# Optimization experiments

Measured on AMD Instinct MI355X. Metric: run time of the kernel, lower is better.

Reference implementation:

```python
import jax, jax.numpy as jnp
import numpy as np
import math

B, C, H, W = 8, 512, 32, 32
NUM_GROUPS = 32
NUM_HEADS = C // 64  # num_head_channels=64 -> 8 heads
EPS = 1e-5


def setup_inputs() -> dict:
    key = jax.random.key(0)
    ks = jax.random.split(key, 7)
    x = jax.random.normal(ks[0], (B, C, H, W), dtype=jnp.float32)
    gn_w = jax.random.uniform(ks[1], (C,), dtype=jnp.float32, minval=0.5, maxval=1.5)
    gn_b = jax.random.normal(ks[2], (C,), dtype=jnp.float32) * 0.1
    qkv_w = jax.random.normal(ks[3], (3 * C, C), dtype=jnp.float32) * 0.02
    qkv_b = jax.random.normal(ks[4], (3 * C,), dtype=jnp.float32) * 0.02
    proj_w = jax.random.normal(ks[5], (C, C), dtype=jnp.float32) * 0.02
    proj_b = jax.random.normal(ks[6], (C,), dtype=jnp.float32) * 0.02
    return {"x": x, "gn_w": gn_w, "gn_b": gn_b, "qkv_w": qkv_w,
            "qkv_b": qkv_b, "proj_w": proj_w, "proj_b": proj_b}


def _group_norm(x, w, b):
    # x: [B, C, L]
    bb, cc, ll = x.shape
    g = x.reshape(bb, NUM_GROUPS, cc // NUM_GROUPS, ll)
    mean = g.mean(axis=(2, 3), keepdims=True)
    var = g.var(axis=(2, 3), keepdims=True)
    g = (g - mean) * jax.lax.rsqrt(var + EPS)
    return g.reshape(bb, cc, ll) * w[None, :, None] + b[None, :, None]


def reference(x, gn_w, gn_b, qkv_w, qkv_b, proj_w, proj_b):
    b, c, h, w = x.shape
    L = h * w
    xf = x.reshape(b, c, L)
    # 1x1 conv1d QKV on normalized input: weight [3C, C]
    qkv = jnp.einsum('oc,bcl->bol', qkv_w, _group_norm(xf, gn_w, gn_b)) + qkv_b[None, :, None]
    ch = c // NUM_HEADS  # per-head channels
    qkv = qkv.reshape(b * NUM_HEADS, 3 * ch, L)
    q, k, v = qkv[:, :ch], qkv[:, ch:2 * ch], qkv[:, 2 * ch:]
    scale = 1.0 / math.sqrt(math.sqrt(ch))
    # [b*H, T, S] scores, softmax over source dim (computed in fp32 per source)
    weight = jnp.einsum('bct,bcs->bts', q * scale, k * scale)
    weight = jax.nn.softmax(weight.astype(jnp.float32), axis=-1).astype(weight.dtype)
    a = jnp.einsum('bts,bcs->bct', weight, v).reshape(b, c, L)
    hproj = jnp.einsum('oc,bcl->bol', proj_w, a) + proj_b[None, :, None]
    return (xf + hproj).reshape(b, c, h, w)
```

## Files before the change

### kernel.cpp

```cpp
#include <hip/hip_runtime.h>
#include <math.h>

#define BB 8
#define CC 512
#define LL 1024
#define GG 32
#define CPG 16
#define NH 8
#define CH 64

typedef unsigned short ushort_t;
typedef __attribute__((ext_vector_type(8))) short short8;
typedef __attribute__((ext_vector_type(4))) float f32x4;
typedef __attribute__((ext_vector_type(16))) float f32x16;

#define SCALE_Q 0.18033688f

__device__ inline ushort_t f2bf(float f) {
  union { float f; unsigned u; } v;
  v.f = f;
  unsigned r = v.u + 0x7FFFu + ((v.u >> 16) & 1u);
  return (ushort_t)(r >> 16);
}

__device__ inline unsigned pack_bf2(float lo, float hi) {
  return __builtin_amdgcn_perm(__float_as_uint(hi), __float_as_uint(lo),
                               0x07060302u);
}

__device__ inline int swz(int r, int k) {
  return r * 64 + ((((k >> 3) ^ (r & 7)) << 3) | (k & 7));
}

__device__ __forceinline__ void g2l16(const void* g, void* l) {
  __builtin_amdgcn_global_load_lds((const unsigned int*)g, (unsigned int*)l,
                                   16, 0, 0);
}

__global__ __launch_bounds__(512) void gnx_kernel(
    const float* __restrict__ x, const float* __restrict__ gn_w,
    const float* __restrict__ gn_b, const float* __restrict__ qkv_w,
    const float* __restrict__ proj_w, ushort_t* __restrict__ xnT,
    ushort_t* __restrict__ wq, ushort_t* __restrict__ wp) {
  if (blockIdx.x < BB * GG) {
    const int b = blockIdx.x / GG;
    const int g = blockIdx.x % GG;
    const int tid = threadIdx.x;
    const int ch = tid >> 5;
    const int lseg = tid & 31;
    __shared__ ushort_t Ts[1024 * 32];
    __shared__ float red[16];
    __shared__ float st[2];
    const float* xc = x + ((size_t)b * CC + (size_t)g * CPG + ch) * LL;
    float4 v[8];
    float sum = 0.f, sq = 0.f;
#pragma unroll
    for (int i = 0; i < 8; ++i) {
      v[i] = *(const float4*)(xc + lseg * 32 + i * 4);
      sum += (v[i].x + v[i].y) + (v[i].z + v[i].w);
      sq += (v[i].x * v[i].x + v[i].y * v[i].y) +
            (v[i].z * v[i].z + v[i].w * v[i].w);
    }
#pragma unroll
    for (int off = 32; off > 0; off >>= 1) {
      sum += __shfl_down(sum, off);
      sq += __shfl_down(sq, off);
    }
    const int wave = tid >> 6;
    if ((tid & 63) == 0) {
      red[wave] = sum;
      red[8 + wave] = sq;
    }
    __syncthreads();
    if (tid == 0) {
      float s = 0.f, q = 0.f;
#pragma unroll
      for (int i = 0; i < 8; ++i) {
        s += red[i];
        q += red[8 + i];
      }
      float mean = s * (1.f / (CPG * LL));
      float var = q * (1.f / (CPG * LL)) - mean * mean;
      st[0] = mean;
      st[1] = rsqrtf(var + 1e-5f);
    }
    __syncthreads();
    const int c = g * CPG + ch;
    const float sc = st[1] * gn_w[c];
    const float sh = gn_b[c] - st[0] * sc;
    const int chG = ch >> 3, ch7 = ch & 7;
#pragma unroll
    for (int i = 0; i < 8; ++i) {
      float vv[4] = {v[i].x, v[i].y, v[i].z, v[i].w};
#pragma unroll
      for (int j = 0; j < 4; ++j) {
        int l = lseg * 32 + i * 4 + j;
        int key = ((l >> 5) + (l >> 2)) & 3;
        int slot = (chG + key) & 3;
        Ts[l * 32 + slot * 8 + ch7] = f2bf(vv[j] * sc + sh);
      }
    }
    __syncthreads();
    const int cb64 = (g >> 2) * 64;
    const int grpb = (g & 3) * 2;
#pragma unroll
    for (int it = 0; it < 4; ++it) {
      int idx = tid + it * 512;
      int l = idx >> 1, gsel = idx & 1;
      int key = ((l >> 5) + (l >> 2)) & 3;
      int slot = (gsel + key) & 3;
      uint4 val = *(const uint4*)&Ts[l * 32 + slot * 8];
      int grp = (grpb + gsel) ^ (l & 7);
      *(uint4*)(xnT + ((size_t)b * LL + l) * CC + cb64 + grp * 8) = val;
    }
  } else {
    int cb = blockIdx.x - BB * GG;
    int idx = (cb * 512 + threadIdx.x) * 4;
    const int N1 = 3 * CC * CC;
    float4 v;
    ushort_t* mat;
    int row, k;
    if (idx < N1) {
      v = *(const float4*)(qkv_w + idx);
      row = idx >> 9;
      k = idx & 511;
      mat = wq + (size_t)row * CC;
    } else {
      int j = idx - N1;
      v = *(const float4*)(proj_w + j);
      row = j >> 9;
      k = j & 511;
      mat = wp + (size_t)row * CC;
    }
    int dcol = (k & ~63) | ((((k >> 3) & 7) ^ (row & 7)) << 3) | (k & 7);
    unsigned lo = f2bf(v.x) | ((unsigned)f2bf(v.y) << 16);
    unsigned hi = f2bf(v.z) | ((unsigned)f2bf(v.w) << 16);
    *(uint2*)(mat + dcol) = make_uint2(lo, hi);
  }
}

__global__ __launch_bounds__(384, 3) void qkv_mfma_kernel(
    const ushort_t* __restrict__ wq, const ushort_t* __restrict__ xnT,
    const float* __restrict__ qkv_b, ushort_t* __restrict__ qT,
    ushort_t* __restrict__ kT, ushort_t* __restrict__ vbuf) {
  const int b = blockIdx.z;
  const int m0 = blockIdx.y * 192;
  const int n0 = blockIdx.x * 128;
  const int tid = threadIdx.x;
  const int w = tid >> 6, lane = tid & 63;
  const int col = lane & 15, quad = lane >> 4;
  const int wm = (w >> 1) * 64, wn = (w & 1) * 64;
  __shared__ ushort_t Smem[2 * 20480];
  f32x4 acc[4][4];
  f32x4 z = {0.f, 0.f, 0.f, 0.f};
#pragma unroll
  for (int i = 0; i < 4; ++i)
#pragma unroll
    for (int j = 0; j < 4; ++j) acc[i][j] = z;

  const ushort_t* arow = wq + (size_t)m0 * CC;
  const ushort_t* brow = xnT + ((size_t)b * LL + n0) * CC;

  auto stage = [&](int bb, int k0) {
    ushort_t* As = Smem + bb * 20480;
    ushort_t* Bs = As + 12288;
#pragma unroll
    for (int j = 0; j < 4; ++j) {
      int e = (j * 6 + w) * 512 + lane * 8;
      g2l16(arow + (size_t)(e >> 6) * CC + k0 + (e & 63),
            As + (j * 6 + w) * 512);
    }
    if (w < 4) {
#pragma unroll
      for (int j = 0; j < 4; ++j) {
        int e = (j * 4 + w) * 512 + lane * 8;
        g2l16(brow + (size_t)(e >> 6) * CC + k0 + (e & 63),
              Bs + (j * 4 + w) * 512);
      }
    }
  };

  stage(0, 0);
  __syncthreads();
  int cur = 0;
  for (int step = 0; step < 8; ++step) {
    if (step < 7) stage(cur ^ 1, (step + 1) * 64);
    const ushort_t* As = Smem + cur * 20480;
    const ushort_t* Bs = As + 12288;
#pragma unroll
    for (int kk = 0; kk < 2; ++kk) {
      short8 af[4], bf[4];
#pragma unroll
      for (int mi = 0; mi < 4; ++mi)
        af[mi] = *(const short8*)&As[swz(wm + mi * 16 + col, kk * 32 + quad * 8)];
#pragma unroll
      for (int ni = 0; ni < 4; ++ni)
        bf[ni] = *(const short8*)&Bs[swz(wn + ni * 16 + col, kk * 32 + quad * 8)];
#pragma unroll
      for (int mi = 0; mi < 4; ++mi)
#pragma unroll
        for (int ni = 0; ni < 4; ++ni)
          acc[mi][ni] = __builtin_amdgcn_mfma_f32_16x16x32_bf16(
              af[mi], bf[ni], acc[mi][ni], 0, 0, 0);
    }
    __syncthreads();
    cur ^= 1;
  }
  const int ci_w = w >> 1;
  ushort_t* Tile = Smem + ci_w * 8192;
  if (ci_w < 2) {
    const float sc = (ci_w == 0) ? SCALE_Q : 1.f;
#pragma unroll
    for (int mi = 0; mi < 4; ++mi) {
      int mg = m0 + wm + mi * 16 + quad * 4;
      float b0 = qkv_b[mg + 0], b1 = qkv_b[mg + 1];
      float b2 = qkv_b[mg + 2], b3 = qkv_b[mg + 3];
      int ch = mi * 16 + quad * 4;
#pragma unroll
      for (int ni = 0; ni < 4; ++ni) {
        int lloc = wn + ni * 16 + col;
        float v0 = (acc[mi][ni][0] + b0) * sc;
        float v1 = (acc[mi][ni][1] + b1) * sc;
        float v2 = (acc[mi][ni][2] + b2) * sc;
        float v3 = (acc[mi][ni][3] + b3) * sc;
        int chs = ch ^ ((lloc & 7) << 3);
        *(uint2*)&Tile[lloc * 64 + chs] =
            make_uint2(pack_bf2(v0, v1), pack_bf2(v2, v3));
      }
    }
  } else {
#pragma unroll
    for (int mi = 0; mi < 4; ++mi)
#pragma unroll
      for (int r = 0; r < 4; ++r) {
        int ch = mi * 16 + quad * 4 + r;
        float bias = qkv_b[m0 + wm + ch];
#pragma unroll
        for (int ni = 0; ni < 4; ++ni) {
          int lloc = wn + ni * 16 + col;
          Tile[ch * 128 + lloc] =
              (ushort_t)(__float_as_uint(acc[mi][ni][r] + bias) >> 16);
        }
      }
  }
  __syncthreads();
  const int head = blockIdx.y;
  const int bh = b * NH + head;
#pragma unroll
  for (int ci = 0; ci < 3; ++ci) {
    ushort_t* T2 = Smem + ci * 8192;
    if (ci < 2) {
      ushort_t* dst = (ci == 0) ? qT : kT;
#pragma unroll
      for (int it = 0; it < 3; ++it) {
        int idx = tid + it * 384;
        if (idx < 1024) {
          int l = idx >> 3, seg = idx & 7;
          uint4 v = *(const uint4*)&T2[l * 64 + seg * 8];
          *(uint4*)(dst + ((size_t)bh * LL + n0 + l) * CH + seg * 8) = v;
        }
      }
    } else {
#pragma unroll
      for (int it = 0; it < 3; ++it) {
        int idx = tid + it * 384;
        if (idx < 1024) {
          int ch = idx >> 4, lseg = idx & 15;
          uint4 v = *(const uint4*)&T2[ch * 128 + lseg * 8];
          int g = lseg & 7, blk = lseg >> 3;
          *(uint4*)(vbuf + ((size_t)bh * CH + ch) * LL + n0 + blk * 64 +
                    ((g ^ (ch & 7)) << 3)) = v;
        }
      }
    }
  }
}

__global__ __launch_bounds__(512) void attn_mfma_kernel(
    const ushort_t* __restrict__ qT, const ushort_t* __restrict__ kT,
    const ushort_t* __restrict__ vbuf, ushort_t* __restrict__ abuf) {
  const int Bx = blockIdx.x;
  const int bh = (Bx & 7) * 8 + ((Bx >> 3) >> 2);
  const int t0g = ((Bx >> 3) & 3) * 256;
  const int b = bh >> 3, h = bh & 7;
  const int tid = threadIdx.x;
  const int w = tid >> 6, lane = tid & 63;
  const int ln31 = lane & 31, hi = lane >> 5;
  __shared__ ushort_t Ksm[2][64 * 64];
  __shared__ ushort_t Vsm[2][64 * 64];

  const ushort_t* kbase = kT + (size_t)bh * LL * CH;
  const ushort_t* vbase = vbuf + (size_t)bh * CH * LL;
  const int eb = w * 512 + lane * 8;

  g2l16(kbase + eb, &Ksm[0][w * 512]);
  g2l16(vbase + (size_t)(eb >> 6) * LL + (eb & 63), &Vsm[0][w * 512]);
  const ushort_t* qtile = qT + ((size_t)bh * LL + t0g) * CH;
  short8 bq[4];
#pragma unroll
  for (int j = 0; j < 4; ++j)
    bq[j] = *(const short8*)&qtile[swz(w * 32 + ln31, j * 16 + hi * 8)];

  float m_s = 0.f, lsum = 0.f;
  f32x16 oacc[2];
  f32x16 zz = {0.f, 0.f, 0.f, 0.f, 0.f, 0.f, 0.f, 0.f,
               0.f, 0.f, 0.f, 0.f, 0.f, 0.f, 0.f, 0.f};
  oacc[0] = zz;
  oacc[1] = zz;
  __syncthreads();

  int cur = 0;
  for (int it = 0; it < 16; ++it) {
    if (it < 15) {
      g2l16(kbase + (size_t)(it + 1) * 64 * CH + eb, &Ksm[cur ^ 1][w * 512]);
      g2l16(vbase + (size_t)(eb >> 6) * LL + (it + 1) * 64 + (eb & 63),
            &Vsm[cur ^ 1][w * 512]);
    }
    const ushort_t* Kc = Ksm[cur];
    const ushort_t* Vc = Vsm[cur];
    f32x16 sacc[2];
    sacc[0] = zz;
    sacc[1] = zz;
    __builtin_amdgcn_s_setprio(1);
#pragma unroll
    for (int sq = 0; sq < 2; ++sq)
#pragma unroll
      for (int j = 0; j < 4; ++j) {
        short8 ak = *(const short8*)&Kc[swz(sq * 32 + ln31, j * 16 + hi * 8)];
        sacc[sq] = __builtin_amdgcn_mfma_f32_32x32x16_bf16(ak, bq[j],
                                                           sacc[sq], 0, 0, 0);
      }
    __builtin_amdgcn_s_setprio(0);
    if (it == 0) {
      float mx = sacc[0][0];
#pragma unroll
      for (int sq = 0; sq < 2; ++sq)
#pragma unroll
        for (int r = 0; r < 16; ++r) mx = fmaxf(mx, sacc[sq][r]);
#pragma unroll
      for (int off = 32; off > 0; off >>= 1) mx = fmaxf(mx, __shfl_xor(mx, off));
      m_s = mx;
    }
    short8 pf[4];
#pragma unroll
    for (int sq = 0; sq < 2; ++sq) {
      float p[16];
#pragma unroll
      for (int r = 0; r < 16; ++r) {
        p[r] = __builtin_amdgcn_exp2f(sacc[sq][r] - m_s);
        lsum += p[r];
      }
      unsigned d0[4], d1[4];
#pragma unroll
      for (int q = 0; q < 4; ++q) {
        d0[q] = pack_bf2(p[q * 4 + 0], p[q * 4 + 1]);
        d1[q] = pack_bf2(p[q * 4 + 2], p[q * 4 + 3]);
      }
#pragma unroll
      for (int m = 0; m < 2; ++m) {
        unsigned x0 = d0[m * 2], y0 = d0[m * 2 + 1];
        unsigned x1 = d1[m * 2], y1 = d1[m * 2 + 1];
        asm volatile("v_permlane32_swap_b32 %0, %1" : "+v"(x0), "+v"(y0));
        asm volatile("v_permlane32_swap_b32 %0, %1" : "+v"(x1), "+v"(y1));
        union { uint4 u; short8 s; } fu;
        fu.u = make_uint4(x0, x1, y0, y1);
        pf[sq * 2 + m] = fu.s;
      }
    }
    __builtin_amdgcn_s_setprio(1);
#pragma unroll
    for (int cq = 0; cq < 2; ++cq)
#pragma unroll
      for (int ks = 0; ks < 4; ++ks) {
        short8 bv = *(const short8*)&Vc[swz(cq * 32 + ln31, ks * 16 + hi * 8)];
        oacc[cq] = __builtin_amdgcn_mfma_f32_32x32x16_bf16(pf[ks], bv,
                                                           oacc[cq], 0, 0, 0);
      }
    __builtin_amdgcn_s_setprio(0);
    __syncthreads();
    cur ^= 1;
  }
  lsum += __shfl_xor(lsum, 32);
#pragma unroll
  for (int r = 0; r < 16; ++r) {
    int tl = (r & 3) + 8 * (r >> 2) + 4 * hi;
    float li = 1.f / __shfl(lsum, tl, 64);
    int lg = t0g + w * 32 + tl;
#pragma unroll
    for (int cq = 0; cq < 2; ++cq) {
      int cl = cq * 32 + ln31;
      int dcol = ((((cl >> 3) ^ (lg & 7)) << 3) | (cl & 7));
      abuf[((size_t)b * LL + lg) * CC + h * CH + dcol] =
          f2bf(oacc[cq][r] * li);
    }
  }
}

__global__ __launch_bounds__(256) void proj_mfma_kernel(
    const ushort_t* __restrict__ wp, const ushort_t* __restrict__ abuf,
    const float* __restrict__ proj_b, const float* __restrict__ x,
    float* __restrict__ out) {
  const int b = blockIdx.z;
  const int m0 = blockIdx.y * 64;
  const int n0 = blockIdx.x * 128;
  const int tid = threadIdx.x;
  const int w = tid >> 6, lane = tid & 63;
  const int col = lane & 15, quad = lane >> 4;
  const int wm = (w >> 1) * 32, wn = (w & 1) * 64;
  __shared__ ushort_t Smem[2 * 12288];
  f32x4 acc[2][4];
  f32x4 z = {0.f, 0.f, 0.f, 0.f};
#pragma unroll
  for (int i = 0; i < 2; ++i)
#pragma unroll
    for (int j = 0; j < 4; ++j) acc[i][j] = z;

  const ushort_t* arow = wp + (size_t)m0 * CC;
  const ushort_t* brow = abuf + ((size_t)b * LL + n0) * CC;

  auto stage = [&](int bb, int k0) {
    ushort_t* As = Smem + bb * 12288;
    ushort_t* Bs = As + 4096;
#pragma unroll
    for (int j = 0; j < 2; ++j) {
      int e = (j * 4 + w) * 512 + lane * 8;
      g2l16(arow + (size_t)(e >> 6) * CC + k0 + (e & 63),
            As + (j * 4 + w) * 512);
    }
#pragma unroll
    for (int j = 0; j < 4; ++j) {
      int e = (j * 4 + w) * 512 + lane * 8;
      g2l16(brow + (size_t)(e >> 6) * CC + k0 + (e & 63),
            Bs + (j * 4 + w) * 512);
    }
  };

  stage(0, 0);
  __syncthreads();
  int cur = 0;
  for (int step = 0; step < 8; ++step) {
    if (step < 7) stage(cur ^ 1, (step + 1) * 64);
    const ushort_t* As = Smem + cur * 12288;
    const ushort_t* Bs = As + 4096;
#pragma unroll
    for (int kk = 0; kk < 2; ++kk) {
      short8 af[2], bf[4];
#pragma unroll
      for (int mi = 0; mi < 2; ++mi)
        af[mi] = *(const short8*)&As[swz(wm + mi * 16 + col, kk * 32 + quad * 8)];
#pragma unroll
      for (int ni = 0; ni < 4; ++ni)
        bf[ni] = *(const short8*)&Bs[swz(wn + ni * 16 + col, kk * 32 + quad * 8)];
#pragma unroll
      for (int mi = 0; mi < 2; ++mi)
#pragma unroll
        for (int ni = 0; ni < 4; ++ni)
          acc[mi][ni] = __builtin_amdgcn_mfma_f32_16x16x32_bf16(
              af[mi], bf[ni], acc[mi][ni], 0, 0, 0);
    }
    __syncthreads();
    cur ^= 1;
  }
#pragma unroll
  for (int mi = 0; mi < 2; ++mi)
#pragma unroll
    for (int r = 0; r < 4; ++r) {
      int o = m0 + wm + mi * 16 + quad * 4 + r;
      float bias = proj_b[o];
#pragma unroll
      for (int ni = 0; ni < 4; ++ni) {
        int l = n0 + wn + ni * 16 + col;
        size_t off = ((size_t)b * CC + o) * LL + l;
        out[off] = x[off] + bias + acc[mi][ni][r];
      }
    }
}

extern "C" void kernel_launch(void* const* d_in, const int* in_sizes, int n_in,
                              void* d_out, int out_size, void* d_ws,
                              size_t ws_size, hipStream_t stream) {
  const float* x = (const float*)d_in[0];
  const float* gn_w = (const float*)d_in[1];
  const float* gn_b = (const float*)d_in[2];
  const float* qkv_w = (const float*)d_in[3];
  const float* qkv_b = (const float*)d_in[4];
  const float* proj_w = (const float*)d_in[5];
  const float* proj_b = (const float*)d_in[6];
  float* out = (float*)d_out;

  char* ws = (char*)d_ws;
  ushort_t* wq = (ushort_t*)ws;
  ushort_t* wp = wq + (size_t)3 * CC * CC;
  ushort_t* xnT = wp + (size_t)CC * CC;
  ushort_t* qT = xnT + (size_t)BB * LL * CC;
  ushort_t* kT = qT + (size_t)BB * NH * LL * CH;
  ushort_t* vb = kT + (size_t)BB * NH * LL * CH;
  ushort_t* abuf = vb + (size_t)BB * NH * LL * CH;

  gnx_kernel<<<BB * GG + 512, 512, 0, stream>>>(x, gn_w, gn_b, qkv_w, proj_w,
                                                xnT, wq, wp);
  qkv_mfma_kernel<<<dim3(LL / 128, 1536 / 192, BB), 384, 0, stream>>>(
      wq, xnT, qkv_b, qT, kT, vb);
  attn_mfma_kernel<<<dim3(256), 512, 0, stream>>>(qT, kT, vb, abuf);
  proj_mfma_kernel<<<dim3(LL / 128, CC / 64, BB), 256, 0, stream>>>(
      wp, abuf, proj_b, x, out);
}
```

Baseline: 140.1 us.

## Retile attention to 128-query blocks with 128-key stages and MFMA row sums

The attention kernel now runs 512 blocks of 4 waves, each covering 128 queries, instead of 256 blocks of 8 waves. Each pipeline stage double-buffers a 128-key K/V tile, so there are half as many barriers per block. V tiles are addressed with a new 128-wide swizzle that matches the existing 64-element swizzle in the V buffer. The softmax denominator is now computed by an extra MFMA against a vector of bf16 ones rather than scalar adds and shuffles. This adds about a quarter more matrix work and doubles global K/V reads per head, in exchange for more blocks, fewer syncs and less VALU work.

```diff
diff --git a/kernel.cpp b/kernel.cpp
--- a/kernel.cpp
+++ b/kernel.cpp
@@ -30,6 +30,10 @@
 
 __device__ inline int swz(int r, int k) {
   return r * 64 + ((((k >> 3) ^ (r & 7)) << 3) | (k & 7));
+}
+
+__device__ inline int vswz(int c, int s) {
+  return c * 128 + (s & 64) + ((((s >> 3) & 7) ^ (c & 7)) << 3) + (s & 7);
 }
 
 __device__ __forceinline__ void g2l16(const void* g, void* l) {
@@ -276,115 +280,137 @@
   }
 }
 
-__global__ __launch_bounds__(512) void attn_mfma_kernel(
+__global__ __launch_bounds__(256) void attn_mfma_kernel(
     const ushort_t* __restrict__ qT, const ushort_t* __restrict__ kT,
     const ushort_t* __restrict__ vbuf, ushort_t* __restrict__ abuf) {
   const int Bx = blockIdx.x;
-  const int bh = (Bx & 7) * 8 + ((Bx >> 3) >> 2);
-  const int t0g = ((Bx >> 3) & 3) * 256;
+  const int bh = (Bx & 7) * 8 + ((Bx >> 3) >> 3);
+  const int t0g = ((Bx >> 3) & 7) * 128;
   const int b = bh >> 3, h = bh & 7;
   const int tid = threadIdx.x;
   const int w = tid >> 6, lane = tid & 63;
   const int ln31 = lane & 31, hi = lane >> 5;
-  __shared__ ushort_t Ksm[2][64 * 64];
-  __shared__ ushort_t Vsm[2][64 * 64];
+  __shared__ ushort_t Ksm[2][128 * 64];
+  __shared__ ushort_t Vsm[2][64 * 128];
 
   const ushort_t* kbase = kT + (size_t)bh * LL * CH;
   const ushort_t* vbase = vbuf + (size_t)bh * CH * LL;
-  const int eb = w * 512 + lane * 8;
-
-  g2l16(kbase + eb, &Ksm[0][w * 512]);
-  g2l16(vbase + (size_t)(eb >> 6) * LL + (eb & 63), &Vsm[0][w * 512]);
+
+#pragma unroll
+  for (int i = 0; i < 4; ++i) {
+    int e = i * 2048 + w * 512 + lane * 8;
+    g2l16(kbase + e, &Ksm[0][i * 2048 + w * 512]);
+    g2l16(vbase + (size_t)(e >> 7) * LL + (e & 127),
+          &Vsm[0][i * 2048 + w * 512]);
+  }
   const ushort_t* qtile = qT + ((size_t)bh * LL + t0g) * CH;
   short8 bq[4];
 #pragma unroll
   for (int j = 0; j < 4; ++j)
     bq[j] = *(const short8*)&qtile[swz(w * 32 + ln31, j * 16 + hi * 8)];
 
-  float m_s = 0.f, lsum = 0.f;
-  f32x16 oacc[2];
+  union { unsigned u[4]; short8 s; } onesu;
+#pragma unroll
+  for (int i = 0; i < 4; ++i) onesu.u[i] = 0x3F803F80u;
+  const short8 bones = onesu.s;
+
+  float m_s = 0.f;
+  f32x16 oacc[2], osum;
   f32x16 zz = {0.f, 0.f, 0.f, 0.f, 0.f, 0.f, 0.f, 0.f,
                0.f, 0.f, 0.f, 0.f, 0.f, 0.f, 0.f, 0.f};
   oacc[0] = zz;
   oacc[1] = zz;
+  osum = zz;
   __syncthreads();
 
   int cur = 0;
-  for (int it = 0; it < 16; ++it) {
-    if (it < 15) {
-      g2l16(kbase + (size_t)(it + 1) * 64 * CH + eb, &Ksm[cur ^ 1][w * 512]);
-      g2l16(vbase + (size_t)(eb >> 6) * LL + (it + 1) * 64 + (eb & 63),
-            &Vsm[cur ^ 1][w * 512]);
+  for (int it2 = 0; it2 < 8; ++it2) {
+    if (it2 < 7) {
+#pragma unroll
+      for (int i = 0; i < 4; ++i) {
+        int e = i * 2048 + w * 512 + lane * 8;
+        g2l16(kbase + (size_t)(it2 + 1) * 8192 + e,
+              &Ksm[cur ^ 1][i * 2048 + w * 512]);
+        g2l16(vbase + (size_t)(e >> 7) * LL + (it2 + 1) * 128 + (e & 127),
+              &Vsm[cur ^ 1][i * 2048 + w * 512]);
+      }
     }
     const ushort_t* Kc = Ksm[cur];
     const ushort_t* Vc = Vsm[cur];
-    f32x16 sacc[2];
-    sacc[0] = zz;
-    sacc[1] = zz;
-    __builtin_amdgcn_s_setprio(1);
-#pragma unroll
-    for (int sq = 0; sq < 2; ++sq)
-#pragma unroll
-      for (int j = 0; j < 4; ++j) {
-        short8 ak = *(const short8*)&Kc[swz(sq * 32 + ln31, j * 16 + hi * 8)];
-        sacc[sq] = __builtin_amdgcn_mfma_f32_32x32x16_bf16(ak, bq[j],
-                                                           sacc[sq], 0, 0, 0);
-      }
-    __builtin_amdgcn_s_setprio(0);
-    if (it == 0) {
-      float mx = sacc[0][0];
+#pragma unroll
+    for (int h2 = 0; h2 < 2; ++h2) {
+      f32x16 sacc[2];
+      sacc[0] = zz;
+      sacc[1] = zz;
+      __builtin_amdgcn_s_setprio(1);
 #pragma unroll
       for (int sq = 0; sq < 2; ++sq)
 #pragma unroll
-        for (int r = 0; r < 16; ++r) mx = fmaxf(mx, sacc[sq][r]);
-#pragma unroll
-      for (int off = 32; off > 0; off >>= 1) mx = fmaxf(mx, __shfl_xor(mx, off));
-      m_s = mx;
-    }
-    short8 pf[4];
-#pragma unroll
-    for (int sq = 0; sq < 2; ++sq) {
-      float p[16];
-#pragma unroll
-      for (int r = 0; r < 16; ++r) {
-        p[r] = __builtin_amdgcn_exp2f(sacc[sq][r] - m_s);
-        lsum += p[r];
-      }
-      unsigned d0[4], d1[4];
-#pragma unroll
-      for (int q = 0; q < 4; ++q) {
-        d0[q] = pack_bf2(p[q * 4 + 0], p[q * 4 + 1]);
-        d1[q] = pack_bf2(p[q * 4 + 2], p[q * 4 + 3]);
-      }
-#pragma unroll
-      for (int m = 0; m < 2; ++m) {
-        unsigned x0 = d0[m * 2], y0 = d0[m * 2 + 1];
-        unsigned x1 = d1[m * 2], y1 = d1[m * 2 + 1];
-        asm volatile("v_permlane32_swap_b32 %0, %1" : "+v"(x0), "+v"(y0));
-        asm volatile("v_permlane32_swap_b32 %0, %1" : "+v"(x1), "+v"(y1));
-        union { uint4 u; short8 s; } fu;
-        fu.u = make_uint4(x0, x1, y0, y1);
-        pf[sq * 2 + m] = fu.s;
-      }
-    }
-    __builtin_amdgcn_s_setprio(1);
-#pragma unroll
-    for (int cq = 0; cq < 2; ++cq)
-#pragma unroll
-      for (int ks = 0; ks < 4; ++ks) {
-        short8 bv = *(const short8*)&Vc[swz(cq * 32 + ln31, ks * 16 + hi * 8)];
-        oacc[cq] = __builtin_amdgcn_mfma_f32_32x32x16_bf16(pf[ks], bv,
-                                                           oacc[cq], 0, 0, 0);
-      }
-    __builtin_amdgcn_s_setprio(0);
+        for (int j = 0; j < 4; ++j) {
+          short8 ak = *(const short8*)&Kc[swz(h2 * 64 + sq * 32 + ln31,
+                                              j * 16 + hi * 8)];
+          sacc[sq] = __builtin_amdgcn_mfma_f32_32x32x16_bf16(ak, bq[j],
+                                                             sacc[sq], 0, 0, 0);
+        }
+      __builtin_amdgcn_s_setprio(0);
+      if (it2 == 0 && h2 == 0) {
+        float mx = sacc[0][0];
+#pragma unroll
+        for (int sq = 0; sq < 2; ++sq)
+#pragma unroll
+          for (int r = 0; r < 16; ++r) mx = fmaxf(mx, sacc[sq][r]);
+#pragma unroll
+        for (int off = 32; off > 0; off >>= 1)
+          mx = fmaxf(mx, __shfl_xor(mx, off));
+        m_s = mx;
+      }
+      short8 pf[4];
+#pragma unroll
+      for (int sq = 0; sq < 2; ++sq) {
+        float p[16];
+#pragma unroll
+        for (int r = 0; r < 16; ++r)
+          p[r] = __builtin_amdgcn_exp2f(sacc[sq][r] - m_s);
+        unsigned d0[4], d1[4];
+#pragma unroll
+        for (int q = 0; q < 4; ++q) {
+          d0[q] = pack_bf2(p[q * 4 + 0], p[q * 4 + 1]);
+          d1[q] = pack_bf2(p[q * 4 + 2], p[q * 4 + 3]);
+        }
+#pragma unroll
+        for (int m = 0; m < 2; ++m) {
+          unsigned x0 = d0[m * 2], y0 = d0[m * 2 + 1];
+          unsigned x1 = d1[m * 2], y1 = d1[m * 2 + 1];
+          asm volatile("v_permlane32_swap_b32 %0, %1" : "+v"(x0), "+v"(y0));
+          asm volatile("v_permlane32_swap_b32 %0, %1" : "+v"(x1), "+v"(y1));
+          union { uint4 u; short8 s; } fu;
+          fu.u = make_uint4(x0, x1, y0, y1);
+          pf[sq * 2 + m] = fu.s;
+        }
+      }
+      __builtin_amdgcn_s_setprio(1);
+#pragma unroll
+      for (int cq = 0; cq < 2; ++cq)
+#pragma unroll
+        for (int ks = 0; ks < 4; ++ks) {
+          short8 bv = *(const short8*)&Vc[vswz(cq * 32 + ln31,
+                                               h2 * 64 + ks * 16 + hi * 8)];
+          oacc[cq] = __builtin_amdgcn_mfma_f32_32x32x16_bf16(pf[ks], bv,
+                                                             oacc[cq], 0, 0, 0);
+        }
+#pragma unroll
+      for (int ks = 0; ks < 4; ++ks)
+        osum = __builtin_amdgcn_mfma_f32_32x32x16_bf16(pf[ks], bones, osum,
+                                                       0, 0, 0);
+      __builtin_amdgcn_s_setprio(0);
+    }
     __syncthreads();
     cur ^= 1;
   }
-  lsum += __shfl_xor(lsum, 32);
 #pragma unroll
   for (int r = 0; r < 16; ++r) {
     int tl = (r & 3) + 8 * (r >> 2) + 4 * hi;
-    float li = 1.f / __shfl(lsum, tl, 64);
+    float li = 1.f / osum[r];
     int lg = t0g + w * 32 + tl;
 #pragma unroll
     for (int cq = 0; cq < 2; ++cq) {
@@ -501,7 +527,7 @@
                                                 xnT, wq, wp);
   qkv_mfma_kernel<<<dim3(LL / 128, 1536 / 192, BB), 384, 0, stream>>>(
       wq, xnT, qkv_b, qT, kT, vb);
-  attn_mfma_kernel<<<dim3(256), 512, 0, stream>>>(qT, kT, vb, abuf);
+  attn_mfma_kernel<<<dim3(512), 256, 0, stream>>>(qT, kT, vb, abuf);
   proj_mfma_kernel<<<dim3(LL / 128, CC / 64, BB), 256, 0, stream>>>(
       wp, abuf, proj_b, x, out);
 }
```

New measurement: 138.5 us (median of 2 runs). No clear change (-1.1%).
